# Kernel tuning notes

Measured on AMD Instinct MI355X. Metric: run time of the kernel, lower is better.

Reference implementation:

```python
import jax, jax.numpy as jnp
import numpy as np

N, C, H = 384, 128, 4

def setup_inputs() -> dict:
    key = jax.random.key(0)
    ks = jax.random.split(key, 8)
    s = 1.0 / np.sqrt(C).astype(np.float32)
    pair = jax.random.normal(ks[0], (N, N, C), jnp.float32)
    mask = (jax.random.uniform(ks[1], (N, N)) > 0.5).astype(jnp.float32)
    return {
        'pair': pair,
        'mask': mask,
        'ln_w': jnp.ones((C,), jnp.float32),
        'ln_b': jnp.zeros((C,), jnp.float32),
        'bias_w': jax.random.normal(ks[2], (H, C), jnp.float32) * s,
        'q_w': jax.random.normal(ks[3], (C, C), jnp.float32) * s,
        'k_w': jax.random.normal(ks[4], (C, C), jnp.float32) * s,
        'v_w': jax.random.normal(ks[5], (C, C), jnp.float32) * s,
        'g_w': jax.random.normal(ks[6], (C, C), jnp.float32) * s,
        'o_w': jax.random.normal(ks[7], (C, C), jnp.float32) * s,
    }

def reference(pair, mask, ln_w, ln_b, bias_w, q_w, k_w, v_w, g_w, o_w):
    n, _, c = pair.shape
    h = bias_w.shape[0]
    d = c // h  # qkv_dim = c_pair // num_head
    # LayerNorm over channel dim (eps=1e-5, torch default)
    mu = jnp.mean(pair, axis=-1, keepdims=True)
    var = jnp.var(pair, axis=-1, keepdims=True)
    x = (pair - mu) * jax.lax.rsqrt(var + 1e-5) * ln_w + ln_b  # [N,N,C]
    # nonbatched pair bias: Linear(C->H), then permute(2,0,1) -> [H,N,N]
    bias = jnp.einsum('ijc,hc->hij', x, bias_w)
    # per-row (b) attention over keys j; Linear weight W: y = x @ W.T
    q = (x @ q_w.T).reshape(n, n, h, d)
    k = (x @ k_w.T).reshape(n, n, h, d)
    v = (x @ v_w.T).reshape(n, n, h, d)
    mask_bias = 1e9 * (mask - 1.0)  # [N,N]: -inf-like where masked per row b, key j
    logits = jnp.einsum('bihd,bjhd->bhij', q, k) * (1.0 / np.sqrt(d).astype(np.float32))
    logits = logits + bias[None, :, :, :] + mask_bias[:, None, None, :]
    w = jax.nn.softmax(logits, axis=-1)  # [N,H,N,N]
    o = jnp.einsum('bhij,bjhd->bihd', w, v).reshape(n, n, c)
    gate = jax.nn.sigmoid(x @ g_w.T)
    return (gate * o) @ o_w.T  # [N,N,C]
```

## Files before the change

kernel.cpp:

```cpp
#include <hip/hip_runtime.h>
#include <hip/hip_bf16.h>

#define NN 384
#define CC 128
#define HH 4
#define DD 32
#define QK_SCALE 0.17677669529663687f

typedef float f32x4 __attribute__((ext_vector_type(4)));
typedef short s16x8 __attribute__((ext_vector_type(8)));
typedef unsigned short u16;

__device__ __forceinline__ u16 f2b(float f) {
  union { float f; unsigned u; } c; c.f = f;
  unsigned u = c.u + 0x7FFFu + ((c.u >> 16) & 1u);
  return (u16)(u >> 16);
}

#define MFMA16(a, b, c) __builtin_amdgcn_mfma_f32_16x16x32_bf16((a), (b), (c), 0, 0, 0)

__global__ __launch_bounds__(256) void k_ln_bias(
    const float* __restrict__ pair, const float* __restrict__ ln_w,
    const float* __restrict__ ln_b, const float* __restrict__ bias_w,
    u16* __restrict__ xb, float* __restrict__ biasb) {
  const int wave = threadIdx.x >> 6;
  const int l = threadIdx.x & 63;
  const int p = blockIdx.x * 4 + wave;

  const float2 v = ((const float2*)pair)[(size_t)p * 64 + l];
  float s = v.x + v.y, sq = v.x * v.x + v.y * v.y;
#pragma unroll
  for (int off = 32; off >= 1; off >>= 1) {
    s += __shfl_xor(s, off);
    sq += __shfl_xor(sq, off);
  }
  const float mean = s * (1.0f / 128.0f);
  const float rstd = rsqrtf(sq * (1.0f / 128.0f) - mean * mean + 1e-5f);
  const float2 lw = ((const float2*)ln_w)[l];
  const float2 lb2 = ((const float2*)ln_b)[l];
  const float x0 = (v.x - mean) * rstd * lw.x + lb2.x;
  const float x1 = (v.y - mean) * rstd * lw.y + lb2.y;
  ((unsigned*)xb)[(size_t)p * 64 + l] =
      (unsigned)f2b(x0) | ((unsigned)f2b(x1) << 16);

#pragma unroll
  for (int h = 0; h < HH; ++h) {
    const float2 bw = ((const float2*)bias_w)[h * 64 + l];
    float bp = x0 * bw.x + x1 * bw.y;
#pragma unroll
    for (int off = 32; off >= 1; off >>= 1) bp += __shfl_xor(bp, off);
    if (l == 0) biasb[(size_t)h * NN * NN + p] = bp;
  }
}

__global__ __launch_bounds__(512) void k_qkv(
    const u16* __restrict__ xb, const float* __restrict__ q_w,
    const float* __restrict__ k_w, const float* __restrict__ v_w,
    u16* __restrict__ qg, u16* __restrict__ kg, u16* __restrict__ vtg) {
  __shared__ u16 wsh[384][136];
  __shared__ u16 xs[128][136];
  const int t = threadIdx.x;
  const int row0 = blockIdx.x * 128;

  for (int idx = t; idx < 384 * 64; idx += 512) {
    const int n = idx >> 6, cp = idx & 63;
    float2 vv;
    if (n < 128) {
      vv = ((const float2*)q_w)[n * 64 + cp];
      vv.x *= QK_SCALE;
      vv.y *= QK_SCALE;
    } else if (n < 256) {
      vv = ((const float2*)k_w)[(n - 128) * 64 + cp];
    } else {
      vv = ((const float2*)v_w)[(n - 256) * 64 + cp];
    }
    ((unsigned*)&wsh[n][0])[cp] =
        (unsigned)f2b(vv.x) | ((unsigned)f2b(vv.y) << 16);
  }
  for (int idx = t; idx < 128 * 64; idx += 512) {
    const int r = idx >> 6, cp = idx & 63;
    ((unsigned*)&xs[r][0])[cp] = ((const unsigned*)xb)[((size_t)row0 + r) * 64 + cp];
  }
  __syncthreads();

  const int w = t >> 6, l = t & 63;
  const int m0 = (w >> 2) * 64, n0 = (w & 3) * 96;
  const int lr = l & 15, lg = l >> 4;

  f32x4 acc[4][6];
#pragma unroll
  for (int ms = 0; ms < 4; ++ms)
#pragma unroll
    for (int ns = 0; ns < 6; ++ns) acc[ms][ns] = (f32x4){0.f, 0.f, 0.f, 0.f};

#pragma unroll
  for (int ks = 0; ks < 4; ++ks) {
    s16x8 a[4], bb[6];
#pragma unroll
    for (int ms = 0; ms < 4; ++ms)
      a[ms] = *(const s16x8*)&xs[m0 + ms * 16 + lr][ks * 32 + lg * 8];
#pragma unroll
    for (int ns = 0; ns < 6; ++ns)
      bb[ns] = *(const s16x8*)&wsh[n0 + ns * 16 + lr][ks * 32 + lg * 8];
#pragma unroll
    for (int ms = 0; ms < 4; ++ms)
#pragma unroll
      for (int ns = 0; ns < 6; ++ns)
        acc[ms][ns] = MFMA16(a[ms], bb[ns], acc[ms][ns]);
  }

  const int b = blockIdx.x / 3;
  const int jbase = (blockIdx.x % 3) * 128;
#pragma unroll
  for (int ms = 0; ms < 4; ++ms) {
    const int jl = jbase + m0 + ms * 16 + lg * 4;
#pragma unroll
    for (int ns = 0; ns < 6; ++ns) {
      const int n = n0 + ns * 16 + lr;
      const int h = (n >> 5) & 3, d = n & 31;
      const size_t bh = (size_t)(b * 4 + h);
      if (n < 256) {
        u16* dst = (n < 128 ? qg : kg) + bh * 384 * 32;
#pragma unroll
        for (int r = 0; r < 4; ++r) dst[(jl + r) * 32 + d] = f2b(acc[ms][ns][r]);
      } else {
        unsigned* dst = (unsigned*)vtg + (bh * 32 + d) * 192;
#pragma unroll
        for (int r = 0; r < 4; r += 2)
          dst[(jl >> 1) + (r >> 1)] = (unsigned)f2b(acc[ms][ns][r]) |
                                      ((unsigned)f2b(acc[ms][ns][r + 1]) << 16);
      }
    }
  }
}

__global__ __launch_bounds__(512) void k_attn(
    const u16* __restrict__ qg, const u16* __restrict__ kg,
    const u16* __restrict__ vtg, const float* __restrict__ biasb,
    const float* __restrict__ mask, float* __restrict__ o_out) {
  __shared__ u16 Ks[384][40];
  __shared__ u16 Vts[32][392];
  __shared__ u16 Ps[8 * 48 * 72];
  __shared__ float mb[NN];

  const int bid = blockIdx.x;
  const int b = bid >> 2, h = bid & 3;
  const size_t bh = (size_t)bid;
  const int t = threadIdx.x, w = t >> 6, l = t & 63;
  const int lr = l & 15, lg = l >> 4;

  const unsigned* ksrc = (const unsigned*)(kg + bh * 12288);
  for (int idx = t; idx < 6144; idx += 512)
    ((unsigned*)&Ks[0][0])[(idx >> 4) * 20 + (idx & 15)] = ksrc[idx];
  {
    const unsigned* vsrc = (const unsigned*)(vtg + bh * 12288);
    const int d = t >> 4;
#pragma unroll
    for (int rep = 0; rep < 12; ++rep) {
      const int jp = (t & 15) + rep * 16;
      ((unsigned*)&Vts[0][0])[d * 196 + jp] = vsrc[d * 192 + jp];
    }
  }
  if (t < NN) mb[t] = 1e9f * (mask[b * NN + t] - 1.0f);

  const int q0 = w * 48;
  s16x8 aQ[3];
#pragma unroll
  for (int ms = 0; ms < 3; ++ms)
    aQ[ms] = *(const s16x8*)(qg + bh * 12288 +
                             ((size_t)(q0 + ms * 16 + lr)) * 32 + lg * 8);
  __syncthreads();

  float mr[3][4], lsum[3][4];
  f32x4 oa[3][2];
#pragma unroll
  for (int ms = 0; ms < 3; ++ms) {
#pragma unroll
    for (int r = 0; r < 4; ++r) {
      mr[ms][r] = -3.0e38f;
      lsum[ms][r] = 0.f;
    }
#pragma unroll
    for (int ns = 0; ns < 2; ++ns) oa[ms][ns] = (f32x4){0.f, 0.f, 0.f, 0.f};
  }

  u16* Pw = &Ps[w * 3456];
  const float* bbase = biasb + (size_t)h * NN * NN;
  const f32x4 zero4 = {0.f, 0.f, 0.f, 0.f};

  for (int kt = 0; kt < 6; ++kt) {
    f32x4 s[3][4];
    s16x8 bK[4];
#pragma unroll
    for (int js = 0; js < 4; ++js)
      bK[js] = *(const s16x8*)&Ks[kt * 64 + js * 16 + lr][lg * 8];
#pragma unroll
    for (int ms = 0; ms < 3; ++ms)
#pragma unroll
      for (int js = 0; js < 4; ++js)
        s[ms][js] = MFMA16(aQ[ms], bK[js], zero4);

    const int jb = kt * 64 + lr;
#pragma unroll
    for (int ms = 0; ms < 3; ++ms) {
      const int i0 = q0 + ms * 16 + lg * 4;
#pragma unroll
      for (int js = 0; js < 4; ++js) {
        const int j = jb + js * 16;
        const float mbj = mb[j];
#pragma unroll
        for (int r = 0; r < 4; ++r)
          s[ms][js][r] += bbase[(size_t)(i0 + r) * NN + j] + mbj;
      }
    }

#pragma unroll
    for (int ms = 0; ms < 3; ++ms) {
#pragma unroll
      for (int r = 0; r < 4; ++r) {
        float tm = fmaxf(fmaxf(s[ms][0][r], s[ms][1][r]),
                         fmaxf(s[ms][2][r], s[ms][3][r]));
        tm = fmaxf(tm, __shfl_xor(tm, 1));
        tm = fmaxf(tm, __shfl_xor(tm, 2));
        tm = fmaxf(tm, __shfl_xor(tm, 4));
        tm = fmaxf(tm, __shfl_xor(tm, 8));
        const float nm = fmaxf(mr[ms][r], tm);
        const float sc = __expf(mr[ms][r] - nm);
        mr[ms][r] = nm;
        float ts = 0.f;
#pragma unroll
        for (int js = 0; js < 4; ++js) {
          const float p = __expf(s[ms][js][r] - nm);
          s[ms][js][r] = p;
          ts += p;
        }
        ts += __shfl_xor(ts, 1);
        ts += __shfl_xor(ts, 2);
        ts += __shfl_xor(ts, 4);
        ts += __shfl_xor(ts, 8);
        lsum[ms][r] = lsum[ms][r] * sc + ts;
        oa[ms][0][r] *= sc;
        oa[ms][1][r] *= sc;
      }
    }

#pragma unroll
    for (int ms = 0; ms < 3; ++ms)
#pragma unroll
      for (int js = 0; js < 4; ++js)
#pragma unroll
        for (int r = 0; r < 4; ++r)
          Pw[(ms * 16 + lg * 4 + r) * 72 + js * 16 + lr] = f2b(s[ms][js][r]);

#pragma unroll
    for (int ks = 0; ks < 2; ++ks) {
      s16x8 pa[3], bv[2];
#pragma unroll
      for (int ms = 0; ms < 3; ++ms)
        pa[ms] = *(const s16x8*)&Pw[(ms * 16 + lr) * 72 + ks * 32 + lg * 8];
#pragma unroll
      for (int ns = 0; ns < 2; ++ns)
        bv[ns] = *(const s16x8*)&Vts[ns * 16 + lr][kt * 64 + ks * 32 + lg * 8];
#pragma unroll
      for (int ms = 0; ms < 3; ++ms)
#pragma unroll
        for (int ns = 0; ns < 2; ++ns)
          oa[ms][ns] = MFMA16(pa[ms], bv[ns], oa[ms][ns]);
    }
  }

#pragma unroll
  for (int ms = 0; ms < 3; ++ms) {
#pragma unroll
    for (int r = 0; r < 4; ++r) {
      const float inv = 1.0f / lsum[ms][r];
      const size_t row = (size_t)b * NN + q0 + ms * 16 + lg * 4 + r;
#pragma unroll
      for (int ns = 0; ns < 2; ++ns)
        o_out[row * CC + h * DD + ns * 16 + lr] = oa[ms][ns][r] * inv;
    }
  }
}

__global__ __launch_bounds__(512) void k_gate_out(
    const u16* __restrict__ xb, const float* __restrict__ g_w,
    const float* __restrict__ o_w, float* __restrict__ io) {
  __shared__ u16 gws[128][136];
  __shared__ u16 ows[128][136];
  __shared__ u16 xs[128][136];
  __shared__ u16 as_[128][136];

  const int t = threadIdx.x;
  const int row0 = blockIdx.x * 128;

  for (int idx = t; idx < 128 * 64; idx += 512) {
    const int n = idx >> 6, cp = idx & 63;
    const float2 g2 = ((const float2*)g_w)[idx];
    const float2 o2 = ((const float2*)o_w)[idx];
    ((unsigned*)&gws[n][0])[cp] =
        (unsigned)f2b(g2.x) | ((unsigned)f2b(g2.y) << 16);
    ((unsigned*)&ows[n][0])[cp] =
        (unsigned)f2b(o2.x) | ((unsigned)f2b(o2.y) << 16);
    ((unsigned*)&xs[n][0])[cp] = ((const unsigned*)xb)[((size_t)row0 + n) * 64 + cp];
  }
  __syncthreads();

  const int w = t >> 6, l = t & 63;
  const int m0 = (w >> 2) * 64, n0 = (w & 3) * 32;
  const int lr = l & 15, lg = l >> 4;

  f32x4 acc[4][2];
#pragma unroll
  for (int ms = 0; ms < 4; ++ms)
#pragma unroll
    for (int ns = 0; ns < 2; ++ns) acc[ms][ns] = (f32x4){0.f, 0.f, 0.f, 0.f};

#pragma unroll
  for (int ks = 0; ks < 4; ++ks) {
    s16x8 a[4], bb[2];
#pragma unroll
    for (int ms = 0; ms < 4; ++ms)
      a[ms] = *(const s16x8*)&xs[m0 + ms * 16 + lr][ks * 32 + lg * 8];
#pragma unroll
    for (int ns = 0; ns < 2; ++ns)
      bb[ns] = *(const s16x8*)&gws[n0 + ns * 16 + lr][ks * 32 + lg * 8];
#pragma unroll
    for (int ms = 0; ms < 4; ++ms)
#pragma unroll
      for (int ns = 0; ns < 2; ++ns)
        acc[ms][ns] = MFMA16(a[ms], bb[ns], acc[ms][ns]);
  }

#pragma unroll
  for (int ms = 0; ms < 4; ++ms) {
#pragma unroll
    for (int ns = 0; ns < 2; ++ns) {
#pragma unroll
      for (int r = 0; r < 4; ++r) {
        const int mloc = m0 + ms * 16 + lg * 4 + r;
        const int gcol = n0 + ns * 16 + lr;
        const float ov = io[((size_t)row0 + mloc) * CC + gcol];
        const float gate = 1.0f / (1.0f + __expf(-acc[ms][ns][r]));
        as_[mloc][gcol] = f2b(gate * ov);
      }
    }
  }
  __syncthreads();

  f32x4 acc2[4][2];
#pragma unroll
  for (int ms = 0; ms < 4; ++ms)
#pragma unroll
    for (int ns = 0; ns < 2; ++ns) acc2[ms][ns] = (f32x4){0.f, 0.f, 0.f, 0.f};

#pragma unroll
  for (int ks = 0; ks < 4; ++ks) {
    s16x8 a[4], bb[2];
#pragma unroll
    for (int ms = 0; ms < 4; ++ms)
      a[ms] = *(const s16x8*)&as_[m0 + ms * 16 + lr][ks * 32 + lg * 8];
#pragma unroll
    for (int ns = 0; ns < 2; ++ns)
      bb[ns] = *(const s16x8*)&ows[n0 + ns * 16 + lr][ks * 32 + lg * 8];
#pragma unroll
    for (int ms = 0; ms < 4; ++ms)
#pragma unroll
      for (int ns = 0; ns < 2; ++ns)
        acc2[ms][ns] = MFMA16(a[ms], bb[ns], acc2[ms][ns]);
  }

#pragma unroll
  for (int ms = 0; ms < 4; ++ms)
#pragma unroll
    for (int ns = 0; ns < 2; ++ns)
#pragma unroll
      for (int r = 0; r < 4; ++r)
        io[((size_t)row0 + m0 + ms * 16 + lg * 4 + r) * CC + n0 + ns * 16 + lr] =
            acc2[ms][ns][r];
}

extern "C" void kernel_launch(void* const* d_in, const int* in_sizes, int n_in,
                              void* d_out, int out_size, void* d_ws,
                              size_t ws_size, hipStream_t stream) {
  const float* pair = (const float*)d_in[0];
  const float* mask = (const float*)d_in[1];
  const float* ln_w = (const float*)d_in[2];
  const float* ln_b = (const float*)d_in[3];
  const float* bias_w = (const float*)d_in[4];
  const float* q_w = (const float*)d_in[5];
  const float* k_w = (const float*)d_in[6];
  const float* v_w = (const float*)d_in[7];
  const float* g_w = (const float*)d_in[8];
  const float* o_w = (const float*)d_in[9];

  char* wsb = (char*)d_ws;
  u16* xb = (u16*)wsb;
  float* biasb = (float*)(wsb + 37748736);
  u16* qg = (u16*)(wsb + 40108032);
  u16* kg = (u16*)(wsb + 77856768);
  u16* vtg = (u16*)(wsb + 115605504);
  float* io = (float*)d_out;

  hipLaunchKernelGGL(k_ln_bias, dim3(NN * NN / 4), dim3(256), 0, stream, pair,
                     ln_w, ln_b, bias_w, xb, biasb);
  hipLaunchKernelGGL(k_qkv, dim3(1152), dim3(512), 0, stream, xb, q_w, k_w,
                     v_w, qg, kg, vtg);
  hipLaunchKernelGGL(k_attn, dim3(NN * HH), dim3(512), 0, stream, qg, kg, vtg,
                     biasb, mask, io);
  hipLaunchKernelGGL(k_gate_out, dim3(1152), dim3(512), 0, stream, xb, g_w,
                     o_w, io);
}
```

Baseline: 554.9 us.

## Rewrite all kernels around register-resident MFMA operands and bf16 intermediates

Weight conversion to bf16 now happens once, in an extra block of the LayerNorm kernel. The pair bias is stored as bf16 instead of fp32. The QKV, attention and gate/output kernels drop shared-memory staging and load MFMA operands straight from global memory, using transposed products with 16x16x16 MFMAs so the softmax probabilities stay in registers instead of going through LDS. Attention is split across twice as many smaller blocks, and gate/out runs both GEMMs per wave with no shared memory. This cuts LDS traffic, barriers and bias bandwidth, at the cost of uncached repeated global reads and reduced bias precision.

Result: slower. 664.9 us (+19.8%).

```diff
diff --git a/kernel.cpp b/kernel.cpp
--- a/kernel.cpp
+++ b/kernel.cpp
@@ -9,20 +9,61 @@
 
 typedef float f32x4 __attribute__((ext_vector_type(4)));
 typedef short s16x8 __attribute__((ext_vector_type(8)));
+typedef short s16x4 __attribute__((ext_vector_type(4)));
 typedef unsigned short u16;
+typedef unsigned int u32;
 
 __device__ __forceinline__ u16 f2b(float f) {
-  union { float f; unsigned u; } c; c.f = f;
-  unsigned u = c.u + 0x7FFFu + ((c.u >> 16) & 1u);
+  union { float f; u32 u; } c; c.f = f;
+  u32 u = c.u + 0x7FFFu + ((c.u >> 16) & 1u);
   return (u16)(u >> 16);
 }
-
-#define MFMA16(a, b, c) __builtin_amdgcn_mfma_f32_16x16x32_bf16((a), (b), (c), 0, 0, 0)
+__device__ __forceinline__ u32 pack2(float a, float b) {
+  return (u32)f2b(a) | ((u32)f2b(b) << 16);
+}
+__device__ __forceinline__ float b2f_lo(u32 u) {
+  union { u32 u; float f; } c; c.u = u << 16; return c.f;
+}
+__device__ __forceinline__ float b2f_hi(u32 u) {
+  union { u32 u; float f; } c; c.u = u & 0xFFFF0000u; return c.f;
+}
+__device__ __forceinline__ s16x4 mk4(u32 a, u32 b) {
+  union { u32 u[2]; s16x4 v; } c; c.u[0] = a; c.u[1] = b; return c.v;
+}
+
+#define MFMA32(a, b, c) __builtin_amdgcn_mfma_f32_16x16x32_bf16((a), (b), (c), 0, 0, 0)
+#define MFMA16(a, b, c) __builtin_amdgcn_mfma_f32_16x16x16bf16_1k((a), (b), (c), 0, 0, 0)
 
 __global__ __launch_bounds__(256) void k_ln_bias(
     const float* __restrict__ pair, const float* __restrict__ ln_w,
     const float* __restrict__ ln_b, const float* __restrict__ bias_w,
-    u16* __restrict__ xb, float* __restrict__ biasb) {
+    const float* __restrict__ q_w, const float* __restrict__ k_w,
+    const float* __restrict__ v_w, const float* __restrict__ g_w,
+    const float* __restrict__ o_w, u16* __restrict__ xb,
+    u16* __restrict__ biasb, u16* __restrict__ wqk, u16* __restrict__ wv,
+    u16* __restrict__ wg, u16* __restrict__ wo) {
+  if (blockIdx.x == 36864) {
+    const int t = threadIdx.x;
+    const float2* q2 = (const float2*)q_w;
+    const float2* k2 = (const float2*)k_w;
+    const float2* v2 = (const float2*)v_w;
+    const float2* g2 = (const float2*)g_w;
+    const float2* o2 = (const float2*)o_w;
+    u32* dq = (u32*)wqk;
+    u32* dk = (u32*)wqk + 8192;
+    u32* dv = (u32*)wv;
+    u32* dg = (u32*)wg;
+    u32* dw = (u32*)wo;
+    for (int i = t; i < 8192; i += 256) {
+      float2 a = q2[i];
+      dq[i] = pack2(a.x * QK_SCALE, a.y * QK_SCALE);
+      a = k2[i]; dk[i] = pack2(a.x, a.y);
+      a = v2[i]; dv[i] = pack2(a.x, a.y);
+      a = g2[i]; dg[i] = pack2(a.x, a.y);
+      a = o2[i]; dw[i] = pack2(a.x, a.y);
+    }
+    return;
+  }
   const int wave = threadIdx.x >> 6;
   const int l = threadIdx.x & 63;
   const int p = blockIdx.x * 4 + wave;
@@ -40,8 +81,7 @@
   const float2 lb2 = ((const float2*)ln_b)[l];
   const float x0 = (v.x - mean) * rstd * lw.x + lb2.x;
   const float x1 = (v.y - mean) * rstd * lw.y + lb2.y;
-  ((unsigned*)xb)[(size_t)p * 64 + l] =
-      (unsigned)f2b(x0) | ((unsigned)f2b(x1) << 16);
+  ((u32*)xb)[(size_t)p * 64 + l] = pack2(x0, x1);
 
 #pragma unroll
   for (int h = 0; h < HH; ++h) {
@@ -49,334 +89,275 @@
     float bp = x0 * bw.x + x1 * bw.y;
 #pragma unroll
     for (int off = 32; off >= 1; off >>= 1) bp += __shfl_xor(bp, off);
-    if (l == 0) biasb[(size_t)h * NN * NN + p] = bp;
-  }
-}
-
-__global__ __launch_bounds__(512) void k_qkv(
-    const u16* __restrict__ xb, const float* __restrict__ q_w,
-    const float* __restrict__ k_w, const float* __restrict__ v_w,
-    u16* __restrict__ qg, u16* __restrict__ kg, u16* __restrict__ vtg) {
-  __shared__ u16 wsh[384][136];
-  __shared__ u16 xs[128][136];
-  const int t = threadIdx.x;
-  const int row0 = blockIdx.x * 128;
-
-  for (int idx = t; idx < 384 * 64; idx += 512) {
-    const int n = idx >> 6, cp = idx & 63;
-    float2 vv;
-    if (n < 128) {
-      vv = ((const float2*)q_w)[n * 64 + cp];
-      vv.x *= QK_SCALE;
-      vv.y *= QK_SCALE;
-    } else if (n < 256) {
-      vv = ((const float2*)k_w)[(n - 128) * 64 + cp];
-    } else {
-      vv = ((const float2*)v_w)[(n - 256) * 64 + cp];
-    }
-    ((unsigned*)&wsh[n][0])[cp] =
-        (unsigned)f2b(vv.x) | ((unsigned)f2b(vv.y) << 16);
-  }
-  for (int idx = t; idx < 128 * 64; idx += 512) {
-    const int r = idx >> 6, cp = idx & 63;
-    ((unsigned*)&xs[r][0])[cp] = ((const unsigned*)xb)[((size_t)row0 + r) * 64 + cp];
-  }
-  __syncthreads();
-
-  const int w = t >> 6, l = t & 63;
-  const int m0 = (w >> 2) * 64, n0 = (w & 3) * 96;
-  const int lr = l & 15, lg = l >> 4;
-
-  f32x4 acc[4][6];
-#pragma unroll
-  for (int ms = 0; ms < 4; ++ms)
-#pragma unroll
-    for (int ns = 0; ns < 6; ++ns) acc[ms][ns] = (f32x4){0.f, 0.f, 0.f, 0.f};
-
-#pragma unroll
-  for (int ks = 0; ks < 4; ++ks) {
-    s16x8 a[4], bb[6];
-#pragma unroll
-    for (int ms = 0; ms < 4; ++ms)
-      a[ms] = *(const s16x8*)&xs[m0 + ms * 16 + lr][ks * 32 + lg * 8];
-#pragma unroll
-    for (int ns = 0; ns < 6; ++ns)
-      bb[ns] = *(const s16x8*)&wsh[n0 + ns * 16 + lr][ks * 32 + lg * 8];
-#pragma unroll
-    for (int ms = 0; ms < 4; ++ms)
-#pragma unroll
-      for (int ns = 0; ns < 6; ++ns)
-        acc[ms][ns] = MFMA16(a[ms], bb[ns], acc[ms][ns]);
-  }
-
-  const int b = blockIdx.x / 3;
-  const int jbase = (blockIdx.x % 3) * 128;
-#pragma unroll
-  for (int ms = 0; ms < 4; ++ms) {
-    const int jl = jbase + m0 + ms * 16 + lg * 4;
-#pragma unroll
-    for (int ns = 0; ns < 6; ++ns) {
-      const int n = n0 + ns * 16 + lr;
-      const int h = (n >> 5) & 3, d = n & 31;
-      const size_t bh = (size_t)(b * 4 + h);
-      if (n < 256) {
-        u16* dst = (n < 128 ? qg : kg) + bh * 384 * 32;
-#pragma unroll
-        for (int r = 0; r < 4; ++r) dst[(jl + r) * 32 + d] = f2b(acc[ms][ns][r]);
-      } else {
-        unsigned* dst = (unsigned*)vtg + (bh * 32 + d) * 192;
-#pragma unroll
-        for (int r = 0; r < 4; r += 2)
-          dst[(jl >> 1) + (r >> 1)] = (unsigned)f2b(acc[ms][ns][r]) |
-                                      ((unsigned)f2b(acc[ms][ns][r + 1]) << 16);
-      }
-    }
-  }
-}
-
-__global__ __launch_bounds__(512) void k_attn(
-    const u16* __restrict__ qg, const u16* __restrict__ kg,
-    const u16* __restrict__ vtg, const float* __restrict__ biasb,
-    const float* __restrict__ mask, float* __restrict__ o_out) {
-  __shared__ u16 Ks[384][40];
-  __shared__ u16 Vts[32][392];
-  __shared__ u16 Ps[8 * 48 * 72];
-  __shared__ float mb[NN];
-
+    if (l == 0) biasb[(size_t)h * NN * NN + p] = f2b(bp);
+  }
+}
+
+__global__ __launch_bounds__(256, 4) void k_qkv(
+    const u16* __restrict__ xb, const u16* __restrict__ wqk,
+    const u16* __restrict__ wv, u16* __restrict__ qg, u16* __restrict__ kg,
+    u16* __restrict__ vtg) {
   const int bid = blockIdx.x;
-  const int b = bid >> 2, h = bid & 3;
-  const size_t bh = (size_t)bid;
+  const int b = bid / 6, jt = bid % 6;
+  const int jrow0 = b * NN + jt * 64;
+  const int jloc0 = jt * 64;
   const int t = threadIdx.x, w = t >> 6, l = t & 63;
   const int lr = l & 15, lg = l >> 4;
 
-  const unsigned* ksrc = (const unsigned*)(kg + bh * 12288);
-  for (int idx = t; idx < 6144; idx += 512)
-    ((unsigned*)&Ks[0][0])[(idx >> 4) * 20 + (idx & 15)] = ksrc[idx];
   {
-    const unsigned* vsrc = (const unsigned*)(vtg + bh * 12288);
-    const int d = t >> 4;
-#pragma unroll
-    for (int rep = 0; rep < 12; ++rep) {
-      const int jp = (t & 15) + rep * 16;
-      ((unsigned*)&Vts[0][0])[d * 196 + jp] = vsrc[d * 192 + jp];
-    }
-  }
-  if (t < NN) mb[t] = 1e9f * (mask[b * NN + t] - 1.0f);
-
-  const int q0 = w * 48;
-  s16x8 aQ[3];
+    const int n0 = w * 64;
+    f32x4 acc[4][4];
+#pragma unroll
+    for (int ns = 0; ns < 4; ++ns)
+#pragma unroll
+      for (int ms = 0; ms < 4; ++ms) acc[ns][ms] = (f32x4){0.f, 0.f, 0.f, 0.f};
+#pragma unroll
+    for (int cs = 0; cs < 8; ++cs) {
+      s16x4 bx[4];
+#pragma unroll
+      for (int ms = 0; ms < 4; ++ms)
+        bx[ms] = *(const s16x4*)&xb[(size_t)(jrow0 + ms * 16 + lr) * CC +
+                                    cs * 16 + lg * 4];
+#pragma unroll
+      for (int ns = 0; ns < 4; ++ns) {
+        const s16x4 aW =
+            *(const s16x4*)&wqk[(n0 + ns * 16 + lr) * CC + cs * 16 + lg * 4];
+#pragma unroll
+        for (int ms = 0; ms < 4; ++ms)
+          acc[ns][ms] = MFMA16(aW, bx[ms], acc[ns][ms]);
+      }
+    }
+    u16* base = (n0 >= 128) ? kg : qg;
+#pragma unroll
+    for (int ns = 0; ns < 4; ++ns) {
+      const int n = n0 + ns * 16 + lg * 4;
+      const int h = (n >> 5) & 3, d = n & 31;
+#pragma unroll
+      for (int ms = 0; ms < 4; ++ms) {
+        u32* dst = (u32*)(base + (size_t)(b * 4 + h) * 12288 +
+                          (jloc0 + ms * 16 + lr) * 32 + d);
+        dst[0] = pack2(acc[ns][ms][0], acc[ns][ms][1]);
+        dst[1] = pack2(acc[ns][ms][2], acc[ns][ms][3]);
+      }
+    }
+  }
+
+  {
+    const int m0 = (w & 1) * 32, n0v = (w >> 1) * 64;
+    f32x4 accv[2][4];
+#pragma unroll
+    for (int ms = 0; ms < 2; ++ms)
+#pragma unroll
+      for (int ns = 0; ns < 4; ++ns) accv[ms][ns] = (f32x4){0.f, 0.f, 0.f, 0.f};
+#pragma unroll
+    for (int cs = 0; cs < 4; ++cs) {
+      s16x8 ax[2], bw[4];
+#pragma unroll
+      for (int ms = 0; ms < 2; ++ms)
+        ax[ms] = *(const s16x8*)&xb[(size_t)(jrow0 + m0 + ms * 16 + lr) * CC +
+                                    cs * 32 + lg * 8];
+#pragma unroll
+      for (int ns = 0; ns < 4; ++ns)
+        bw[ns] =
+            *(const s16x8*)&wv[(n0v + ns * 16 + lr) * CC + cs * 32 + lg * 8];
+#pragma unroll
+      for (int ms = 0; ms < 2; ++ms)
+#pragma unroll
+        for (int ns = 0; ns < 4; ++ns)
+          accv[ms][ns] = MFMA32(ax[ms], bw[ns], accv[ms][ns]);
+    }
+#pragma unroll
+    for (int ms = 0; ms < 2; ++ms) {
+#pragma unroll
+      for (int ns = 0; ns < 4; ++ns) {
+        const int n = n0v + ns * 16 + lr;
+        const int h = n >> 5, d = n & 31;
+        const int j = jloc0 + m0 + ms * 16 + lg * 4;
+        u32* dst = (u32*)(vtg + (size_t)(b * 4 + h) * 12288 + d * NN + j);
+        dst[0] = pack2(accv[ms][ns][0], accv[ms][ns][1]);
+        dst[1] = pack2(accv[ms][ns][2], accv[ms][ns][3]);
+      }
+    }
+  }
+}
+
+__global__ __launch_bounds__(256, 3) void k_attn(
+    const u16* __restrict__ qg, const u16* __restrict__ kg,
+    const u16* __restrict__ vtg, const u16* __restrict__ biasb,
+    const float* __restrict__ mask, float* __restrict__ io) {
+  __shared__ float mb[NN];
+  const int bid = blockIdx.x;
+  const int bh = bid >> 1, half = bid & 1;
+  const int b = bh >> 2, h = bh & 3;
+  const int t = threadIdx.x, w = t >> 6, l = t & 63;
+  const int lr = l & 15, lg = l >> 4;
+
+  for (int i = t; i < NN; i += 256) mb[i] = 1e9f * (mask[b * NN + i] - 1.0f);
+  __syncthreads();
+
+  const int q0 = half * 192 + w * 48;
+  const u16* qb = qg + (size_t)bh * 12288;
+  const u16* kb = kg + (size_t)bh * 12288;
+  const u16* vb = vtg + (size_t)bh * 12288;
+  const u16* bb = biasb + (size_t)h * NN * NN;
+
+  s16x8 bQ[3];
 #pragma unroll
   for (int ms = 0; ms < 3; ++ms)
-    aQ[ms] = *(const s16x8*)(qg + bh * 12288 +
-                             ((size_t)(q0 + ms * 16 + lr)) * 32 + lg * 8);
-  __syncthreads();
-
-  float mr[3][4], lsum[3][4];
+    bQ[ms] = *(const s16x8*)&qb[(q0 + ms * 16 + lr) * 32 + lg * 8];
+
+  float mr[3], ls[3];
   f32x4 oa[3][2];
 #pragma unroll
   for (int ms = 0; ms < 3; ++ms) {
-#pragma unroll
-    for (int r = 0; r < 4; ++r) {
-      mr[ms][r] = -3.0e38f;
-      lsum[ms][r] = 0.f;
-    }
-#pragma unroll
-    for (int ns = 0; ns < 2; ++ns) oa[ms][ns] = (f32x4){0.f, 0.f, 0.f, 0.f};
-  }
-
-  u16* Pw = &Ps[w * 3456];
-  const float* bbase = biasb + (size_t)h * NN * NN;
-  const f32x4 zero4 = {0.f, 0.f, 0.f, 0.f};
+    mr[ms] = -3.0e38f;
+    ls[ms] = 0.f;
+    oa[ms][0] = (f32x4){0.f, 0.f, 0.f, 0.f};
+    oa[ms][1] = (f32x4){0.f, 0.f, 0.f, 0.f};
+  }
+  const f32x4 z4 = {0.f, 0.f, 0.f, 0.f};
 
   for (int kt = 0; kt < 6; ++kt) {
-    f32x4 s[3][4];
-    s16x8 bK[4];
+    s16x8 aK[4];
 #pragma unroll
     for (int js = 0; js < 4; ++js)
-      bK[js] = *(const s16x8*)&Ks[kt * 64 + js * 16 + lr][lg * 8];
+      aK[js] = *(const s16x8*)&kb[(kt * 64 + js * 16 + lr) * 32 + lg * 8];
+
+    f32x4 sT[3][4];
 #pragma unroll
     for (int ms = 0; ms < 3; ++ms)
 #pragma unroll
+      for (int js = 0; js < 4; ++js) sT[ms][js] = MFMA32(aK[js], bQ[ms], z4);
+
+#pragma unroll
+    for (int js = 0; js < 4; ++js) {
+      const int jb = kt * 64 + js * 16 + lg * 4;
+      const f32x4 m4 = *(const f32x4*)&mb[jb];
+#pragma unroll
+      for (int ms = 0; ms < 3; ++ms) {
+        const u32* bp = (const u32*)&bb[(size_t)(q0 + ms * 16 + lr) * NN + jb];
+        const u32 b0 = bp[0], b1 = bp[1];
+        sT[ms][js][0] += b2f_lo(b0) + m4[0];
+        sT[ms][js][1] += b2f_hi(b0) + m4[1];
+        sT[ms][js][2] += b2f_lo(b1) + m4[2];
+        sT[ms][js][3] += b2f_hi(b1) + m4[3];
+      }
+    }
+
+    u32 pk[3][4][2];
+#pragma unroll
+    for (int ms = 0; ms < 3; ++ms) {
+      float tm = -3.0e38f;
+#pragma unroll
       for (int js = 0; js < 4; ++js)
-        s[ms][js] = MFMA16(aQ[ms], bK[js], zero4);
-
-    const int jb = kt * 64 + lr;
-#pragma unroll
-    for (int ms = 0; ms < 3; ++ms) {
-      const int i0 = q0 + ms * 16 + lg * 4;
-#pragma unroll
-      for (int js = 0; js < 4; ++js) {
-        const int j = jb + js * 16;
-        const float mbj = mb[j];
-#pragma unroll
-        for (int r = 0; r < 4; ++r)
-          s[ms][js][r] += bbase[(size_t)(i0 + r) * NN + j] + mbj;
-      }
-    }
-
-#pragma unroll
-    for (int ms = 0; ms < 3; ++ms) {
-#pragma unroll
-      for (int r = 0; r < 4; ++r) {
-        float tm = fmaxf(fmaxf(s[ms][0][r], s[ms][1][r]),
-                         fmaxf(s[ms][2][r], s[ms][3][r]));
-        tm = fmaxf(tm, __shfl_xor(tm, 1));
-        tm = fmaxf(tm, __shfl_xor(tm, 2));
-        tm = fmaxf(tm, __shfl_xor(tm, 4));
-        tm = fmaxf(tm, __shfl_xor(tm, 8));
-        const float nm = fmaxf(mr[ms][r], tm);
-        const float sc = __expf(mr[ms][r] - nm);
-        mr[ms][r] = nm;
-        float ts = 0.f;
-#pragma unroll
-        for (int js = 0; js < 4; ++js) {
-          const float p = __expf(s[ms][js][r] - nm);
-          s[ms][js][r] = p;
+#pragma unroll
+        for (int r = 0; r < 4; ++r) tm = fmaxf(tm, sT[ms][js][r]);
+      tm = fmaxf(tm, __shfl_xor(tm, 16));
+      tm = fmaxf(tm, __shfl_xor(tm, 32));
+      const float nm = fmaxf(mr[ms], tm);
+      const float sc = __expf(mr[ms] - nm);
+      mr[ms] = nm;
+      float ts = 0.f;
+#pragma unroll
+      for (int js = 0; js < 4; ++js)
+#pragma unroll
+        for (int r = 0; r < 4; ++r) {
+          const float p = __expf(sT[ms][js][r] - nm);
+          sT[ms][js][r] = p;
           ts += p;
         }
-        ts += __shfl_xor(ts, 1);
-        ts += __shfl_xor(ts, 2);
-        ts += __shfl_xor(ts, 4);
-        ts += __shfl_xor(ts, 8);
-        lsum[ms][r] = lsum[ms][r] * sc + ts;
-        oa[ms][0][r] *= sc;
-        oa[ms][1][r] *= sc;
-      }
-    }
-
-#pragma unroll
-    for (int ms = 0; ms < 3; ++ms)
-#pragma unroll
-      for (int js = 0; js < 4; ++js)
-#pragma unroll
-        for (int r = 0; r < 4; ++r)
-          Pw[(ms * 16 + lg * 4 + r) * 72 + js * 16 + lr] = f2b(s[ms][js][r]);
-
-#pragma unroll
-    for (int ks = 0; ks < 2; ++ks) {
-      s16x8 pa[3], bv[2];
-#pragma unroll
-      for (int ms = 0; ms < 3; ++ms)
-        pa[ms] = *(const s16x8*)&Pw[(ms * 16 + lr) * 72 + ks * 32 + lg * 8];
+      ts += __shfl_xor(ts, 16);
+      ts += __shfl_xor(ts, 32);
+      ls[ms] = ls[ms] * sc + ts;
+      oa[ms][0] *= sc;
+      oa[ms][1] *= sc;
+#pragma unroll
+      for (int js = 0; js < 4; ++js) {
+        pk[ms][js][0] = pack2(sT[ms][js][0], sT[ms][js][1]);
+        pk[ms][js][1] = pack2(sT[ms][js][2], sT[ms][js][3]);
+      }
+    }
+
+#pragma unroll
+    for (int st = 0; st < 4; ++st) {
+      const int jb = kt * 64 + st * 16 + lg * 4;
+      s16x4 aV[2];
 #pragma unroll
       for (int ns = 0; ns < 2; ++ns)
-        bv[ns] = *(const s16x8*)&Vts[ns * 16 + lr][kt * 64 + ks * 32 + lg * 8];
-#pragma unroll
-      for (int ms = 0; ms < 3; ++ms)
+        aV[ns] = *(const s16x4*)&vb[(ns * 16 + lr) * NN + jb];
+#pragma unroll
+      for (int ms = 0; ms < 3; ++ms) {
+        const s16x4 pb = mk4(pk[ms][st][0], pk[ms][st][1]);
 #pragma unroll
         for (int ns = 0; ns < 2; ++ns)
-          oa[ms][ns] = MFMA16(pa[ms], bv[ns], oa[ms][ns]);
+          oa[ms][ns] = MFMA16(aV[ns], pb, oa[ms][ns]);
+      }
     }
   }
 
 #pragma unroll
   for (int ms = 0; ms < 3; ++ms) {
-#pragma unroll
-    for (int r = 0; r < 4; ++r) {
-      const float inv = 1.0f / lsum[ms][r];
-      const size_t row = (size_t)b * NN + q0 + ms * 16 + lg * 4 + r;
-#pragma unroll
-      for (int ns = 0; ns < 2; ++ns)
-        o_out[row * CC + h * DD + ns * 16 + lr] = oa[ms][ns][r] * inv;
-    }
-  }
-}
-
-__global__ __launch_bounds__(512) void k_gate_out(
-    const u16* __restrict__ xb, const float* __restrict__ g_w,
-    const float* __restrict__ o_w, float* __restrict__ io) {
-  __shared__ u16 gws[128][136];
-  __shared__ u16 ows[128][136];
-  __shared__ u16 xs[128][136];
-  __shared__ u16 as_[128][136];
-
-  const int t = threadIdx.x;
-  const int row0 = blockIdx.x * 128;
-
-  for (int idx = t; idx < 128 * 64; idx += 512) {
-    const int n = idx >> 6, cp = idx & 63;
-    const float2 g2 = ((const float2*)g_w)[idx];
-    const float2 o2 = ((const float2*)o_w)[idx];
-    ((unsigned*)&gws[n][0])[cp] =
-        (unsigned)f2b(g2.x) | ((unsigned)f2b(g2.y) << 16);
-    ((unsigned*)&ows[n][0])[cp] =
-        (unsigned)f2b(o2.x) | ((unsigned)f2b(o2.y) << 16);
-    ((unsigned*)&xs[n][0])[cp] = ((const unsigned*)xb)[((size_t)row0 + n) * 64 + cp];
-  }
-  __syncthreads();
-
-  const int w = t >> 6, l = t & 63;
-  const int m0 = (w >> 2) * 64, n0 = (w & 3) * 32;
+    const float inv = 1.0f / ls[ms];
+    float* orow = io + ((size_t)b * NN + q0 + ms * 16 + lr) * CC + h * DD;
+#pragma unroll
+    for (int ns = 0; ns < 2; ++ns) {
+      f32x4 vo = oa[ms][ns];
+      vo *= inv;
+      *(f32x4*)&orow[ns * 16 + lg * 4] = vo;
+    }
+  }
+}
+
+__global__ __launch_bounds__(256, 4) void k_gate_out(
+    const u16* __restrict__ xb, const u16* __restrict__ wg,
+    const u16* __restrict__ wo, float* __restrict__ io) {
+  const int bid = blockIdx.x;
+  const int t = threadIdx.x, w = t >> 6, l = t & 63;
   const int lr = l & 15, lg = l >> 4;
-
-  f32x4 acc[4][2];
-#pragma unroll
-  for (int ms = 0; ms < 4; ++ms)
-#pragma unroll
-    for (int ns = 0; ns < 2; ++ns) acc[ms][ns] = (f32x4){0.f, 0.f, 0.f, 0.f};
-
-#pragma unroll
-  for (int ks = 0; ks < 4; ++ks) {
-    s16x8 a[4], bb[2];
-#pragma unroll
-    for (int ms = 0; ms < 4; ++ms)
-      a[ms] = *(const s16x8*)&xs[m0 + ms * 16 + lr][ks * 32 + lg * 8];
-#pragma unroll
-    for (int ns = 0; ns < 2; ++ns)
-      bb[ns] = *(const s16x8*)&gws[n0 + ns * 16 + lr][ks * 32 + lg * 8];
-#pragma unroll
-    for (int ms = 0; ms < 4; ++ms)
-#pragma unroll
-      for (int ns = 0; ns < 2; ++ns)
-        acc[ms][ns] = MFMA16(a[ms], bb[ns], acc[ms][ns]);
-  }
-
-#pragma unroll
-  for (int ms = 0; ms < 4; ++ms) {
-#pragma unroll
-    for (int ns = 0; ns < 2; ++ns) {
-#pragma unroll
-      for (int r = 0; r < 4; ++r) {
-        const int mloc = m0 + ms * 16 + lg * 4 + r;
-        const int gcol = n0 + ns * 16 + lr;
-        const float ov = io[((size_t)row0 + mloc) * CC + gcol];
-        const float gate = 1.0f / (1.0f + __expf(-acc[ms][ns][r]));
-        as_[mloc][gcol] = f2b(gate * ov);
-      }
-    }
-  }
-  __syncthreads();
-
-  f32x4 acc2[4][2];
-#pragma unroll
-  for (int ms = 0; ms < 4; ++ms)
-#pragma unroll
-    for (int ns = 0; ns < 2; ++ns) acc2[ms][ns] = (f32x4){0.f, 0.f, 0.f, 0.f};
-
-#pragma unroll
-  for (int ks = 0; ks < 4; ++ks) {
-    s16x8 a[4], bb[2];
-#pragma unroll
-    for (int ms = 0; ms < 4; ++ms)
-      a[ms] = *(const s16x8*)&as_[m0 + ms * 16 + lr][ks * 32 + lg * 8];
-#pragma unroll
-    for (int ns = 0; ns < 2; ++ns)
-      bb[ns] = *(const s16x8*)&ows[n0 + ns * 16 + lr][ks * 32 + lg * 8];
-#pragma unroll
-    for (int ms = 0; ms < 4; ++ms)
-#pragma unroll
-      for (int ns = 0; ns < 2; ++ns)
-        acc2[ms][ns] = MFMA16(a[ms], bb[ns], acc2[ms][ns]);
-  }
-
-#pragma unroll
-  for (int ms = 0; ms < 4; ++ms)
-#pragma unroll
-    for (int ns = 0; ns < 2; ++ns)
-#pragma unroll
-      for (int r = 0; r < 4; ++r)
-        io[((size_t)row0 + m0 + ms * 16 + lg * 4 + r) * CC + n0 + ns * 16 + lr] =
-            acc2[ms][ns][r];
+  const int m0g = bid * 64 + w * 16;
+
+  f32x4 a1[8];
+#pragma unroll
+  for (int ns = 0; ns < 8; ++ns) a1[ns] = (f32x4){0.f, 0.f, 0.f, 0.f};
+#pragma unroll
+  for (int cs = 0; cs < 8; ++cs) {
+    const s16x4 bx =
+        *(const s16x4*)&xb[(size_t)(m0g + lr) * CC + cs * 16 + lg * 4];
+#pragma unroll
+    for (int ns = 0; ns < 8; ++ns) {
+      const s16x4 aW =
+          *(const s16x4*)&wg[(ns * 16 + lr) * CC + cs * 16 + lg * 4];
+      a1[ns] = MFMA16(aW, bx, a1[ns]);
+    }
+  }
+
+  s16x4 pk2[8];
+#pragma unroll
+  for (int ns = 0; ns < 8; ++ns) {
+    const int gc = ns * 16 + lg * 4;
+    const f32x4 ov = *(const f32x4*)&io[(size_t)(m0g + lr) * CC + gc];
+    float av[4];
+#pragma unroll
+    for (int r = 0; r < 4; ++r)
+      av[r] = ov[r] / (1.0f + __expf(-a1[ns][r]));
+    pk2[ns] = mk4(pack2(av[0], av[1]), pack2(av[2], av[3]));
+  }
+
+  f32x4 a2[8];
+#pragma unroll
+  for (int ns = 0; ns < 8; ++ns) a2[ns] = (f32x4){0.f, 0.f, 0.f, 0.f};
+#pragma unroll
+  for (int cs = 0; cs < 8; ++cs) {
+#pragma unroll
+    for (int ns = 0; ns < 8; ++ns) {
+      const s16x4 aW =
+          *(const s16x4*)&wo[(ns * 16 + lr) * CC + cs * 16 + lg * 4];
+      a2[ns] = MFMA16(aW, pk2[cs], a2[ns]);
+    }
+  }
+#pragma unroll
+  for (int ns = 0; ns < 8; ++ns)
+    *(f32x4*)&io[(size_t)(m0g + lr) * CC + ns * 16 + lg * 4] = a2[ns];
 }
 
 extern "C" void kernel_launch(void* const* d_in, const int* in_sizes, int n_in,
@@ -395,18 +376,23 @@
 
   char* wsb = (char*)d_ws;
   u16* xb = (u16*)wsb;
-  float* biasb = (float*)(wsb + 37748736);
-  u16* qg = (u16*)(wsb + 40108032);
-  u16* kg = (u16*)(wsb + 77856768);
-  u16* vtg = (u16*)(wsb + 115605504);
+  u16* biasb = (u16*)(wsb + 37748736);
+  u16* wqk = (u16*)(wsb + 38928384);
+  u16* wv = (u16*)(wsb + 38993920);
+  u16* wg = (u16*)(wsb + 39026688);
+  u16* wo = (u16*)(wsb + 39059456);
+  u16* qg = (u16*)(wsb + 39092224);
+  u16* kg = (u16*)(wsb + 76840960);
+  u16* vtg = (u16*)(wsb + 114589696);
   float* io = (float*)d_out;
 
-  hipLaunchKernelGGL(k_ln_bias, dim3(NN * NN / 4), dim3(256), 0, stream, pair,
-                     ln_w, ln_b, bias_w, xb, biasb);
-  hipLaunchKernelGGL(k_qkv, dim3(1152), dim3(512), 0, stream, xb, q_w, k_w,
-                     v_w, qg, kg, vtg);
-  hipLaunchKernelGGL(k_attn, dim3(NN * HH), dim3(512), 0, stream, qg, kg, vtg,
-                     biasb, mask, io);
-  hipLaunchKernelGGL(k_gate_out, dim3(1152), dim3(512), 0, stream, xb, g_w,
-                     o_w, io);
-}
+  hipLaunchKernelGGL(k_ln_bias, dim3(NN * NN / 4 + 1), dim3(256), 0, stream,
+                     pair, ln_w, ln_b, bias_w, q_w, k_w, v_w, g_w, o_w, xb,
+                     biasb, wqk, wv, wg, wo);
+  hipLaunchKernelGGL(k_qkv, dim3(NN * 6), dim3(256), 0, stream, xb, wqk, wv,
+                     qg, kg, vtg);
+  hipLaunchKernelGGL(k_attn, dim3(NN * HH * 2), dim3(256), 0, stream, qg, kg,
+                     vtg, biasb, mask, io);
+  hipLaunchKernelGGL(k_gate_out, dim3(NN * NN / 64), dim3(256), 0, stream, xb,
+                     g_w ? wg : wg, wo, io);
+}
```
